# Optimization experiments

Measured on AMD Instinct MI355X. Metric: run time of the kernel, lower is better.

## Reference

```python
import jax, jax.numpy as jnp
import numpy as np

B, H, T, K, V = 2, 8, 2048, 128, 128


def setup_inputs() -> dict:
    key = jax.random.key(0)
    k1, k2, k3, k4, k5 = jax.random.split(key, 5)
    return {
        "q": jax.random.normal(k1, (B, H, T, K), dtype=jnp.float32),
        "k": jax.random.normal(k2, (B, H, T, K), dtype=jnp.float32),
        "v": jax.random.normal(k3, (B, H, T, V), dtype=jnp.float32),
        "i_gate": jax.random.normal(k4, (B, H, T), dtype=jnp.float32),
        "f_gate": jax.random.normal(k5, (B, H, T), dtype=jnp.float32),
    }


def reference(q, k, v, i_gate, f_gate):
    # Stabilized parallel mLSTM (same math as the chunked Triton kernel,
    # expressed in natural-log base instead of base-2).
    Bq, Hq, Tq, Kd = q.shape
    scale = Kd ** -0.5
    logf = jax.nn.log_sigmoid(f_gate)                      # [B,H,T]
    fc = jnp.cumsum(logf, axis=-1)                         # cumulative forget logits
    # log decay matrix: logD[t,s] = i[s] + (fc[t] - fc[s]) for s <= t
    logD = fc[..., :, None] - fc[..., None, :] + i_gate[..., None, :]  # [B,H,T,T]
    mask = jnp.tril(jnp.ones((Tq, Tq), dtype=bool))
    logD_masked = jnp.where(mask, logD, -jnp.inf)
    m = jnp.max(logD_masked, axis=-1)                      # row-wise stabilizer [B,H,T]
    D = jnp.where(mask, jnp.exp(logD - m[..., None]), 0.0) # stabilized decay matrix
    S = jnp.einsum("bhtk,bhsk->bhts", q, k) * scale * D    # gated scores
    norm = jnp.maximum(jnp.abs(jnp.sum(S, axis=-1)), jnp.exp(-m))  # [B,H,T]
    h = jnp.einsum("bhts,bhsv->bhtv", S, v) / norm[..., None]
    return h
```

## Files before the change

kernel.cpp:

```cpp
#include <hip/hip_runtime.h>

#define T_SEQ 2048
#define DHEAD 128
#define NBH 16
#define SCALE 0.08838834764831845f

typedef unsigned short u16;
typedef unsigned int u32;
typedef u16 u16x4 __attribute__((ext_vector_type(4)));
typedef u16 u16x8 __attribute__((ext_vector_type(8)));
typedef u32 u32x2 __attribute__((ext_vector_type(2)));
typedef short s16x4 __attribute__((ext_vector_type(4)));
typedef __bf16 bf16x8 __attribute__((ext_vector_type(8)));
typedef float f32x4 __attribute__((ext_vector_type(4)));

#define SFENCE() __builtin_amdgcn_sched_barrier(0)

__device__ __forceinline__ u16 f2bfu(float x) {
  union { float f; unsigned u; } c; c.f = x;
  unsigned u = c.u;
  u = u + 0x7FFFu + ((u >> 16) & 1u);
  return (u16)(u >> 16);
}

__device__ __forceinline__ bf16x8 ldsFrag(const u16* p) {
  u16x8 t = *(const u16x8*)p;
  return __builtin_bit_cast(bf16x8, t);
}

__device__ __forceinline__ f32x4 mfma16x16x16bf16(s16x4 a, s16x4 b, f32x4 c) {
#if __has_builtin(__builtin_amdgcn_mfma_f32_16x16x16bf16_1k)
  return __builtin_amdgcn_mfma_f32_16x16x16bf16_1k(a, b, c, 0, 0, 0);
#else
  asm("v_mfma_f32_16x16x16_bf16 %0, %1, %2, %0" : "+v"(c) : "v"(a), "v"(b));
  return c;
#endif
}

__device__ __forceinline__ void gld_lds16(const void* g, void* l) {
  __builtin_amdgcn_global_load_lds(
      (__attribute__((address_space(1))) const unsigned int*)g,
      (__attribute__((address_space(3))) unsigned int*)l, 16, 0, 0);
}

__global__ __launch_bounds__(1024) void gate_scan_kernel(
    const float* __restrict__ ig, const float* __restrict__ fg,
    float* __restrict__ a_out, float* __restrict__ c_out,
    float* __restrict__ fc_out)
{
  const int bh = blockIdx.x, tid = threadIdx.x;
  const int w = tid >> 6, lane = tid & 63;
  const int base = bh * T_SEQ + tid * 2;
  __shared__ float wsum[16];
  __shared__ float wmax[16];

  const float x0 = fg[base], x1 = fg[base + 1];
  const float ls0 = fminf(x0, 0.f) - log1pf(expf(-fabsf(x0)));
  const float ls1 = fminf(x1, 0.f) - log1pf(expf(-fabsf(x1)));
  const float s = ls0 + ls1;

  float sc = s;
#pragma unroll
  for (int off = 1; off < 64; off <<= 1) {
    const float t = __shfl_up(sc, off, 64);
    if (lane >= off) sc += t;
  }
  if (lane == 63) wsum[w] = sc;
  __syncthreads();
  float wo = 0.f;
#pragma unroll
  for (int i = 0; i < 15; ++i) if (i < w) wo += wsum[i];
  const float excl = wo + (sc - s);
  const float fc0 = excl + ls0;
  const float fc1 = excl + ls0 + ls1;
  fc_out[base] = fc0; fc_out[base + 1] = fc1;
  const float a0 = ig[base] - fc0;
  const float a1 = ig[base + 1] - fc1;
  a_out[base] = a0; a_out[base + 1] = a1;

  const float m = fmaxf(a0, a1);
  float mc = m;
#pragma unroll
  for (int off = 1; off < 64; off <<= 1) {
    const float t = __shfl_up(mc, off, 64);
    if (lane >= off) mc = fmaxf(mc, t);
  }
  if (lane == 63) wmax[w] = mc;
  __syncthreads();
  float wmo = -INFINITY;
#pragma unroll
  for (int i = 0; i < 15; ++i) if (i < w) wmo = fmaxf(wmo, wmax[i]);
  const float prev = __shfl_up(mc, 1, 64);
  float exclm = (lane > 0) ? prev : -INFINITY;
  exclm = fmaxf(exclm, wmo);
  c_out[base] = fmaxf(exclm, a0);
  c_out[base + 1] = fmaxf(exclm, m);
}

__global__ __launch_bounds__(256) void cvt_kv_kernel(
    const float* __restrict__ kk, const float* __restrict__ v,
    const float* __restrict__ ag, const float* __restrict__ cg,
    u16* __restrict__ kbf, u16* __restrict__ vt)
{
  const int bh = blockIdx.y, kt = blockIdx.x, tid = threadIdx.x;
  {
    const int r = tid >> 2;
    const int c0 = (tid & 3) * 32;
    const int row = kt * 64 + r;
    const float sc = __expf(ag[bh * T_SEQ + row] - cg[bh * T_SEQ + (row | 63)]);
    const float* sp = kk + ((size_t)bh * T_SEQ + row) * DHEAD + c0;
    u16* dp = kbf + ((size_t)bh * T_SEQ + row) * DHEAD + c0;
#pragma unroll
    for (int j = 0; j < 8; ++j) {
      const float4 x = *(const float4*)(sp + j * 4);
      u16x4 pq;
      pq[0] = f2bfu(x.x * sc); pq[1] = f2bfu(x.y * sc);
      pq[2] = f2bfu(x.z * sc); pq[3] = f2bfu(x.w * sc);
      *(u16x4*)(dp + j * 4) = pq;
    }
  }
  __shared__ __align__(16) u16 L[128 * 72];
  const int n0 = (tid & 31) * 4, k0 = (tid >> 5) * 8;
  const float* vp = v + ((size_t)bh * T_SEQ + kt * 64 + k0) * DHEAD + n0;
  u16 tv[4][8];
#pragma unroll
  for (int rr = 0; rr < 8; ++rr) {
    const float4 x = *(const float4*)(vp + rr * DHEAD);
    tv[0][rr] = f2bfu(x.x); tv[1][rr] = f2bfu(x.y);
    tv[2][rr] = f2bfu(x.z); tv[3][rr] = f2bfu(x.w);
  }
#pragma unroll
  for (int j = 0; j < 4; ++j) {
    u16x8 pq;
#pragma unroll
    for (int rr = 0; rr < 8; ++rr) pq[rr] = tv[j][rr];
    *(u16x8*)(&L[(n0 + j) * 72 + k0]) = pq;
  }
  __syncthreads();
  const int row = tid >> 1, s0 = (tid & 1) * 32;
  u16* op = vt + ((size_t)bh * DHEAD + row) * T_SEQ + kt * 64 + s0;
#pragma unroll
  for (int i = 0; i < 4; ++i)
    *(u16x8*)(op + i * 8) = *(const u16x8*)(&L[row * 72 + s0 + i * 8]);
}

template <bool FAST>
__global__ __launch_bounds__(1024, 4) void mlstm_fwd_kernel(
    const float* __restrict__ qg, const float* __restrict__ kxg,
    const float* __restrict__ vg,
    const u16* __restrict__ kbf, const u16* __restrict__ vtbf,
    const float* __restrict__ ag, const float* __restrict__ cg,
    const float* __restrict__ fcg, float* __restrict__ out)
{
  const int bx = (int)blockIdx.x;
  const int bh = bx & 15, p = bx >> 4;
  const int tid = (int)threadIdx.x;
  const int w = tid >> 6, lane = tid & 63;
  const int quad = lane >> 4, l16 = lane & 15;
  const int kg = w & 3, rq = w >> 2;

  const int qtA = 31 - p, qtB = p;
  const int nA = qtA + 1;

  __shared__ __align__(16) unsigned char SM[133120];
  u16* Kst = (u16*)SM;
  float* osh = (float*)(SM + 98304);
  float* rsh = (float*)(SM + 132096);

  const size_t hoff = (size_t)bh * T_SEQ * DHEAD;
  const int goff = bh * T_SEQ;

  auto barL = [&]() {
    asm volatile("s_waitcnt lgkmcnt(0)" ::: "memory");
    SFENCE();
    __builtin_amdgcn_s_barrier();
    SFENCE();
  };

  bf16x8 qf[4];
  auto loadQ = [&](int lqt) {
    const float* qp = qg + hoff + (size_t)(lqt * 64 + rq * 16 + l16) * DHEAD + quad * 8;
#pragma unroll
    for (int kc = 0; kc < 4; ++kc) {
      const float4 x0 = *(const float4*)(qp + kc * 32);
      const float4 x1 = *(const float4*)(qp + kc * 32 + 4);
      u16x8 t;
      t[0] = f2bfu(x0.x); t[1] = f2bfu(x0.y); t[2] = f2bfu(x0.z); t[3] = f2bfu(x0.w);
      t[4] = f2bfu(x1.x); t[5] = f2bfu(x1.y); t[6] = f2bfu(x1.z); t[7] = f2bfu(x1.w);
      qf[kc] = __builtin_bit_cast(bf16x8, t);
    }
  };

  f32x4 oa[8];
  float rsacc;
  auto zeroAcc = [&]() {
#pragma unroll
    for (int mt = 0; mt < 8; ++mt) oa[mt] = (f32x4){0.f, 0.f, 0.f, 0.f};
    rsacc = 0.f;
  };
  zeroAcc();

  const int skey = tid >> 4, sdb = (tid & 15) ^ (skey & 7);
  const u16* ksBase = kbf + (size_t)goff * DHEAD + (size_t)skey * DHEAD + sdb * 8;
  const int svn = tid >> 3, svk = (tid & 7) ^ (svn & 7);
  const u16* vsBase = vtbf + (size_t)bh * DHEAD * T_SEQ + (size_t)svn * T_SEQ + svk * 8;

  auto stage = [&](int st, int slot) {
    u16* KbL = Kst + slot * 16384;
    u16* VbL = Kst + slot * 16384 + 8192;
    if (FAST) {
      gld_lds16(ksBase + (size_t)st * 64 * DHEAD, KbL + w * 512);
      gld_lds16(vsBase + st * 64, VbL + w * 512);
    } else {
      const float ct = cg[goff + st * 64 + 63];
      const float* kp = kxg + hoff + (size_t)(st * 64) * DHEAD;
      const float* vp = vg + hoff + (size_t)(st * 64) * DHEAD;
      { const float scv = __expf(ag[goff + st * 64 + skey] - ct);
        const float4 x0 = *(const float4*)(kp + (size_t)skey * DHEAD + sdb * 8);
        const float4 x1 = *(const float4*)(kp + (size_t)skey * DHEAD + sdb * 8 + 4);
        u16x8 pk;
        pk[0] = f2bfu(x0.x * scv); pk[1] = f2bfu(x0.y * scv);
        pk[2] = f2bfu(x0.z * scv); pk[3] = f2bfu(x0.w * scv);
        pk[4] = f2bfu(x1.x * scv); pk[5] = f2bfu(x1.y * scv);
        pk[6] = f2bfu(x1.z * scv); pk[7] = f2bfu(x1.w * scv);
        *(u16x8*)(KbL + tid * 8) = pk; }
      { u16x8 pw;
#pragma unroll
        for (int rr = 0; rr < 8; ++rr)
          pw[rr] = f2bfu(vp[(size_t)(svk * 8 + rr) * DHEAD + svn]);
        *(u16x8*)(VbL + tid * 8) = pw; }
    }
  };
  auto stageSeq = [&](int seq, int slot) {
    stage(seq < nA ? seq : seq - nA, slot);
  };

  const int keyA = kg * 16 + l16;
  const int ksw  = l16 & 7;
  const int kbu  = kg * 2 + (quad >> 1);
  const int vbase = l16 * 64 + ((kbu ^ (l16 & 7)) * 8) + (quad & 1) * 4;

  auto computeStage = [&](int cqt, int st, int slot, float ccmax) {
    const u16* KbL = Kst + slot * 16384;
    const u16* VbL = Kst + slot * 16384 + 8192;

    f32x4 sa = (f32x4){0.f, 0.f, 0.f, 0.f};
#pragma unroll
    for (int kc = 0; kc < 4; ++kc) {
      const bf16x8 kf = ldsFrag(KbL + keyA * 128 + (((kc * 4 + quad) ^ ksw) * 8));
      sa = __builtin_amdgcn_mfma_f32_16x16x32_bf16(kf, qf[kc], sa, 0, 0, 0);
    }

    const float etile = SCALE * __expf(cg[goff + st * 64 + 63] - ccmax);
    float x0 = sa[0] * etile, x1 = sa[1] * etile;
    float x2 = sa[2] * etile, x3 = sa[3] * etile;
    if (st == cqt) {
      const int qr = rq * 16 + l16, kb0 = kg * 16 + quad * 4;
      if (kb0 + 0 > qr) x0 = 0.f;
      if (kb0 + 1 > qr) x1 = 0.f;
      if (kb0 + 2 > qr) x2 = 0.f;
      if (kb0 + 3 > qr) x3 = 0.f;
    }
    rsacc += (x0 + x1) + (x2 + x3);
    u32 plo, phi;
    asm("v_cvt_pk_bf16_f32 %0, %1, %2" : "=v"(plo) : "v"(x0), "v"(x1));
    asm("v_cvt_pk_bf16_f32 %0, %1, %2" : "=v"(phi) : "v"(x2), "v"(x3));
    const s16x4 pfr = __builtin_bit_cast(s16x4, (u32x2){plo, phi});

#pragma unroll
    for (int mt = 0; mt < 8; ++mt) {
      const s16x4 va = *(const s16x4*)(VbL + vbase + mt * 1024);
      oa[mt] = mfma16x16x16bf16(va, pfr, oa[mt]);
    }
  };

  auto epilogue = [&](int eqt, float ecmax) {
    float x = rsacc;
    x += __shfl_xor(x, 16, 64);
    x += __shfl_xor(x, 32, 64);
    if (lane < 16) rsh[kg * 64 + rq * 16 + lane] = x;
    barL();
    float inv = 0.f;
    if (kg == 3) {
      const int row = rq * 16 + l16;
      const float tot = rsh[row] + rsh[64 + row] + rsh[128 + row] + rsh[192 + row];
      const float nf = __expf(-(ecmax + fcg[goff + eqt * 64 + row]));
      inv = 1.f / fmaxf(fabsf(tot), nf);
    }
    for (int r = 0; r < 4; ++r) {
      if (kg == r) {
        const int row = rq * 16 + l16;
#pragma unroll
        for (int mt = 0; mt < 8; ++mt) {
          float* ap = osh + row * 132 + mt * 16 + quad * 4;
          f32x4 vv = oa[mt];
          if (r > 0) vv = vv + *(const f32x4*)ap;
          if (r == 3) vv = vv * inv;
          *(f32x4*)ap = vv;
        }
      }
      barL();
    }
    const int col = tid & 31, r0 = tid >> 5;
#pragma unroll
    for (int i = 0; i < 2; ++i) {
      const int row = r0 + 32 * i;
      const f32x4 vv = *(const f32x4*)(osh + row * 132 + col * 4);
      *(f32x4*)(out + hoff + (size_t)(eqt * 64 + row) * DHEAD + col * 4) = vv;
    }
  };

  int qt = qtA;
  float cmax = cg[goff + qtA * 64 + 63];
  loadQ(qtA);
  stageSeq(0, 0);
  stageSeq(1, 1);

  int sl = 0;
  for (int s = 0; s < 33; ++s) {
    if (s < 32) { asm volatile("s_waitcnt vmcnt(2)" ::: "memory"); }
    else        { asm volatile("s_waitcnt vmcnt(0)" ::: "memory"); }
    if (!FAST)  { asm volatile("s_waitcnt lgkmcnt(0)" ::: "memory"); }
    SFENCE();
    __builtin_amdgcn_s_barrier();
    SFENCE();

    if (s + 2 < 33) {
      const int sl2 = (sl >= 1) ? sl - 1 : 2;
      stageSeq(s + 2, sl2);
    }
    const int stq = (s < nA) ? s : s - nA;
    computeStage(qt, stq, sl, cmax);

    if (s == nA - 1) {
      loadQ(qtB);
      epilogue(qtA, cmax);
      zeroAcc();
      qt = qtB;
      cmax = cg[goff + qtB * 64 + 63];
    }
    sl = (sl == 2) ? 0 : sl + 1;
  }
  epilogue(qtB, cmax);
}

extern "C" void kernel_launch(void* const* d_in, const int* in_sizes, int n_in,
                              void* d_out, int out_size, void* d_ws, size_t ws_size,
                              hipStream_t stream) {
  const float* q  = (const float*)d_in[0];
  const float* k  = (const float*)d_in[1];
  const float* v  = (const float*)d_in[2];
  const float* ig = (const float*)d_in[3];
  const float* fg = (const float*)d_in[4];

  const size_t gate_bytes = (size_t)3 * NBH * T_SEQ * sizeof(float);
  const size_t kv_elems   = (size_t)NBH * T_SEQ * DHEAD;
  const bool fast = ws_size >= gate_bytes + 2 * kv_elems * sizeof(u16);

  float* a_ws  = (float*)d_ws;
  float* c_ws  = a_ws + NBH * T_SEQ;
  float* fc_ws = c_ws + NBH * T_SEQ;
  u16* kbf  = (u16*)((char*)d_ws + gate_bytes);
  u16* vtbf = kbf + kv_elems;

  gate_scan_kernel<<<dim3(NBH), dim3(1024), 0, stream>>>(ig, fg, a_ws, c_ws, fc_ws);
  if (fast) {
    cvt_kv_kernel<<<dim3(T_SEQ / 64, NBH), dim3(256), 0, stream>>>(
        k, v, a_ws, c_ws, kbf, vtbf);
    mlstm_fwd_kernel<true><<<dim3(256), dim3(1024), 0, stream>>>(
        q, k, v, kbf, vtbf, a_ws, c_ws, fc_ws, (float*)d_out);
  } else {
    mlstm_fwd_kernel<false><<<dim3(256), dim3(1024), 0, stream>>>(
        q, k, v, kbf, vtbf, a_ws, c_ws, fc_ws, (float*)d_out);
  }
}
```

Before: 146.8 us.

## Restructure K/V staging into double-buffered pairs with one barrier per pair

Replaces the three-slot rolling pipeline, which had a hand-tuned vmcnt wait and barrier per tile, with a ping-pong scheme that stages two key/value tiles per buffer and syncs once per pair. This halves the number of block-wide barriers in the main loop. Shared memory grows to four tile slots, so the output staging buffer is shrunk to 64 columns and the epilogue writes in two halves, which adds barriers there. The explicit waitcnt and sched_barrier control is dropped in favour of __syncthreads, so the compiler may insert more conservative waits and overlap global loads less.

```diff
diff --git a/kernel.cpp b/kernel.cpp
--- a/kernel.cpp
+++ b/kernel.cpp
@@ -13,8 +13,6 @@
 typedef short s16x4 __attribute__((ext_vector_type(4)));
 typedef __bf16 bf16x8 __attribute__((ext_vector_type(8)));
 typedef float f32x4 __attribute__((ext_vector_type(4)));
-
-#define SFENCE() __builtin_amdgcn_sched_barrier(0)
 
 __device__ __forceinline__ u16 f2bfu(float x) {
   union { float f; unsigned u; } c; c.f = x;
@@ -160,22 +158,15 @@
   const int kg = w & 3, rq = w >> 2;
 
   const int qtA = 31 - p, qtB = p;
-  const int nA = qtA + 1;
-
-  __shared__ __align__(16) unsigned char SM[133120];
+  const int nA = qtA + 1, nB = qtB + 1;
+
+  __shared__ __align__(16) unsigned char SM[148992];
   u16* Kst = (u16*)SM;
-  float* osh = (float*)(SM + 98304);
-  float* rsh = (float*)(SM + 132096);
+  float* osh = (float*)(SM + 131072);
+  float* rsh = (float*)(SM + 147968);
 
   const size_t hoff = (size_t)bh * T_SEQ * DHEAD;
   const int goff = bh * T_SEQ;
-
-  auto barL = [&]() {
-    asm volatile("s_waitcnt lgkmcnt(0)" ::: "memory");
-    SFENCE();
-    __builtin_amdgcn_s_barrier();
-    SFENCE();
-  };
 
   bf16x8 qf[4];
   auto loadQ = [&](int lqt) {
@@ -231,8 +222,9 @@
         *(u16x8*)(VbL + tid * 8) = pw; }
     }
   };
-  auto stageSeq = [&](int seq, int slot) {
-    stage(seq < nA ? seq : seq - nA, slot);
+  auto stagePair = [&](int s0, int lim, int pr) {
+    if (s0 < lim)     stage(s0,     pr * 2);
+    if (s0 + 1 < lim) stage(s0 + 1, pr * 2 + 1);
   };
 
   const int keyA = kg * 16 + l16;
@@ -279,7 +271,7 @@
     x += __shfl_xor(x, 16, 64);
     x += __shfl_xor(x, 32, 64);
     if (lane < 16) rsh[kg * 64 + rq * 16 + lane] = x;
-    barL();
+    __syncthreads();
     float inv = 0.f;
     if (kg == 3) {
       const int row = rq * 16 + l16;
@@ -287,61 +279,56 @@
       const float nf = __expf(-(ecmax + fcg[goff + eqt * 64 + row]));
       inv = 1.f / fmaxf(fabsf(tot), nf);
     }
-    for (int r = 0; r < 4; ++r) {
-      if (kg == r) {
-        const int row = rq * 16 + l16;
-#pragma unroll
-        for (int mt = 0; mt < 8; ++mt) {
-          float* ap = osh + row * 132 + mt * 16 + quad * 4;
-          f32x4 vv = oa[mt];
-          if (r > 0) vv = vv + *(const f32x4*)ap;
-          if (r == 3) vv = vv * inv;
-          *(f32x4*)ap = vv;
+    const int srow = tid >> 4, scol = tid & 15;
+#pragma unroll
+    for (int h = 0; h < 2; ++h) {
+      for (int r = 0; r < 4; ++r) {
+        if (kg == r) {
+          const int row = rq * 16 + l16;
+#pragma unroll
+          for (int ml = 0; ml < 4; ++ml) {
+            float* ap = osh + row * 66 + ml * 16 + quad * 4;
+            f32x4 vv = oa[h * 4 + ml];
+            if (r > 0) vv = vv + *(const f32x4*)ap;
+            if (r == 3) vv = vv * inv;
+            *(f32x4*)ap = vv;
+          }
         }
+        __syncthreads();
       }
-      barL();
-    }
-    const int col = tid & 31, r0 = tid >> 5;
-#pragma unroll
-    for (int i = 0; i < 2; ++i) {
-      const int row = r0 + 32 * i;
-      const f32x4 vv = *(const f32x4*)(osh + row * 132 + col * 4);
-      *(f32x4*)(out + hoff + (size_t)(eqt * 64 + row) * DHEAD + col * 4) = vv;
-    }
-  };
-
-  int qt = qtA;
+      {
+        const f32x4 vv = *(const f32x4*)(osh + srow * 66 + scol * 4);
+        *(f32x4*)(out + hoff + (size_t)(eqt * 64 + srow) * DHEAD + h * 64 + scol * 4) = vv;
+      }
+      __syncthreads();
+    }
+  };
+
+  int qt = qtA, n = nA;
   float cmax = cg[goff + qtA * 64 + 63];
   loadQ(qtA);
-  stageSeq(0, 0);
-  stageSeq(1, 1);
-
-  int sl = 0;
-  for (int s = 0; s < 33; ++s) {
-    if (s < 32) { asm volatile("s_waitcnt vmcnt(2)" ::: "memory"); }
-    else        { asm volatile("s_waitcnt vmcnt(0)" ::: "memory"); }
-    if (!FAST)  { asm volatile("s_waitcnt lgkmcnt(0)" ::: "memory"); }
-    SFENCE();
-    __builtin_amdgcn_s_barrier();
-    SFENCE();
-
-    if (s + 2 < 33) {
-      const int sl2 = (sl >= 1) ? sl - 1 : 2;
-      stageSeq(s + 2, sl2);
-    }
-    const int stq = (s < nA) ? s : s - nA;
-    computeStage(qt, stq, sl, cmax);
-
-    if (s == nA - 1) {
-      loadQ(qtB);
-      epilogue(qtA, cmax);
+  stagePair(0, nA, 0);
+  __syncthreads();
+
+  int pr = 0;
+  for (int phase = 0; phase < 2; ++phase) {
+    const int c = (n + 1) >> 1;
+    for (int g = 0; g < c; ++g) {
+      if (g + 1 < c)        stagePair(2 * (g + 1), n, pr ^ 1);
+      else if (phase == 0)  stagePair(0, nB, pr ^ 1);
+      computeStage(qt, 2 * g, pr * 2, cmax);
+      if (2 * g + 1 < n) computeStage(qt, 2 * g + 1, pr * 2 + 1, cmax);
+      __syncthreads();
+      pr ^= 1;
+    }
+    if (phase == 0) loadQ(qtB);
+    epilogue(qt, cmax);
+    if (phase == 0) {
       zeroAcc();
-      qt = qtB;
+      qt = qtB; n = nB;
       cmax = cg[goff + qtB * 64 + 63];
     }
-    sl = (sl == 2) ? 0 : sl + 1;
-  }
-  epilogue(qtB, cmax);
+  }
 }
 
 extern "C" void kernel_launch(void* const* d_in, const int* in_sizes, int n_in,
```

After: 154.9 us. +5.5%, slower.

## Read V fragments directly from global memory and double-buffer only K in LDS

Applied to the files above, without the earlier changes.

Stops staging V tiles through LDS. Each wave now loads its V^T fragments straight from global memory inside the PV MFMA loop, and the K pipeline drops from a 3-slot to a 2-slot double buffer with plain __syncthreads, which halves LDS use per block. Per-tile cumulative gate values are preloaded into a register once and fetched with wave shuffles instead of repeated global loads. The intent is to cut LDS footprint and staging traffic. The cost is exposed global-load latency on the V path, since it is no longer prefetched, and a less pipelined barrier schedule.

```diff
diff --git a/kernel.cpp b/kernel.cpp
--- a/kernel.cpp
+++ b/kernel.cpp
@@ -13,8 +13,6 @@
 typedef short s16x4 __attribute__((ext_vector_type(4)));
 typedef __bf16 bf16x8 __attribute__((ext_vector_type(8)));
 typedef float f32x4 __attribute__((ext_vector_type(4)));
-
-#define SFENCE() __builtin_amdgcn_sched_barrier(0)
 
 __device__ __forceinline__ u16 f2bfu(float x) {
   union { float f; unsigned u; } c; c.f = x;
@@ -162,20 +160,15 @@
   const int qtA = 31 - p, qtB = p;
   const int nA = qtA + 1;
 
-  __shared__ __align__(16) unsigned char SM[133120];
+  __shared__ __align__(16) unsigned char SM[67584];
   u16* Kst = (u16*)SM;
-  float* osh = (float*)(SM + 98304);
-  float* rsh = (float*)(SM + 132096);
+  float* osh = (float*)(SM + 32768);
+  float* rsh = (float*)(SM + 66560);
 
   const size_t hoff = (size_t)bh * T_SEQ * DHEAD;
   const int goff = bh * T_SEQ;
 
-  auto barL = [&]() {
-    asm volatile("s_waitcnt lgkmcnt(0)" ::: "memory");
-    SFENCE();
-    __builtin_amdgcn_s_barrier();
-    SFENCE();
-  };
+  const float cgl = cg[goff + (lane & 31) * 64 + 63];
 
   bf16x8 qf[4];
   auto loadQ = [&](int lqt) {
@@ -202,47 +195,33 @@
 
   const int skey = tid >> 4, sdb = (tid & 15) ^ (skey & 7);
   const u16* ksBase = kbf + (size_t)goff * DHEAD + (size_t)skey * DHEAD + sdb * 8;
-  const int svn = tid >> 3, svk = (tid & 7) ^ (svn & 7);
-  const u16* vsBase = vtbf + (size_t)bh * DHEAD * T_SEQ + (size_t)svn * T_SEQ + svk * 8;
-
-  auto stage = [&](int st, int slot) {
-    u16* KbL = Kst + slot * 16384;
-    u16* VbL = Kst + slot * 16384 + 8192;
+
+  auto stage = [&](int st, int b) {
+    u16* KbL = Kst + b * 8192;
     if (FAST) {
       gld_lds16(ksBase + (size_t)st * 64 * DHEAD, KbL + w * 512);
-      gld_lds16(vsBase + st * 64, VbL + w * 512);
     } else {
       const float ct = cg[goff + st * 64 + 63];
-      const float* kp = kxg + hoff + (size_t)(st * 64) * DHEAD;
-      const float* vp = vg + hoff + (size_t)(st * 64) * DHEAD;
-      { const float scv = __expf(ag[goff + st * 64 + skey] - ct);
-        const float4 x0 = *(const float4*)(kp + (size_t)skey * DHEAD + sdb * 8);
-        const float4 x1 = *(const float4*)(kp + (size_t)skey * DHEAD + sdb * 8 + 4);
-        u16x8 pk;
-        pk[0] = f2bfu(x0.x * scv); pk[1] = f2bfu(x0.y * scv);
-        pk[2] = f2bfu(x0.z * scv); pk[3] = f2bfu(x0.w * scv);
-        pk[4] = f2bfu(x1.x * scv); pk[5] = f2bfu(x1.y * scv);
-        pk[6] = f2bfu(x1.z * scv); pk[7] = f2bfu(x1.w * scv);
-        *(u16x8*)(KbL + tid * 8) = pk; }
-      { u16x8 pw;
-#pragma unroll
-        for (int rr = 0; rr < 8; ++rr)
-          pw[rr] = f2bfu(vp[(size_t)(svk * 8 + rr) * DHEAD + svn]);
-        *(u16x8*)(VbL + tid * 8) = pw; }
-    }
-  };
-  auto stageSeq = [&](int seq, int slot) {
-    stage(seq < nA ? seq : seq - nA, slot);
+      const float* kp = kxg + hoff + (size_t)(st * 64 + skey) * DHEAD + sdb * 8;
+      const float scv = __expf(ag[goff + st * 64 + skey] - ct);
+      const float4 x0 = *(const float4*)kp;
+      const float4 x1 = *(const float4*)(kp + 4);
+      u16x8 pk;
+      pk[0] = f2bfu(x0.x * scv); pk[1] = f2bfu(x0.y * scv);
+      pk[2] = f2bfu(x0.z * scv); pk[3] = f2bfu(x0.w * scv);
+      pk[4] = f2bfu(x1.x * scv); pk[5] = f2bfu(x1.y * scv);
+      pk[6] = f2bfu(x1.z * scv); pk[7] = f2bfu(x1.w * scv);
+      *(u16x8*)(KbL + tid * 8) = pk;
+    }
   };
 
   const int keyA = kg * 16 + l16;
   const int ksw  = l16 & 7;
-  const int kbu  = kg * 2 + (quad >> 1);
-  const int vbase = l16 * 64 + ((kbu ^ (l16 & 7)) * 8) + (quad & 1) * 4;
-
-  auto computeStage = [&](int cqt, int st, int slot, float ccmax) {
-    const u16* KbL = Kst + slot * 16384;
-    const u16* VbL = Kst + slot * 16384 + 8192;
+  const u16* vTh = vtbf + (size_t)bh * DHEAD * T_SEQ + (size_t)l16 * T_SEQ
+                 + kg * 16 + quad * 4;
+
+  auto computeStage = [&](int cqt, int st, int b, float ccmax) {
+    const u16* KbL = Kst + b * 8192;
 
     f32x4 sa = (f32x4){0.f, 0.f, 0.f, 0.f};
 #pragma unroll
@@ -251,7 +230,8 @@
       sa = __builtin_amdgcn_mfma_f32_16x16x32_bf16(kf, qf[kc], sa, 0, 0, 0);
     }
 
-    const float etile = SCALE * __expf(cg[goff + st * 64 + 63] - ccmax);
+    const float ct = __shfl(cgl, st, 64);
+    const float etile = SCALE * __expf(ct - ccmax);
     float x0 = sa[0] * etile, x1 = sa[1] * etile;
     float x2 = sa[2] * etile, x3 = sa[3] * etile;
     if (st == cqt) {
@@ -267,9 +247,21 @@
     asm("v_cvt_pk_bf16_f32 %0, %1, %2" : "=v"(phi) : "v"(x2), "v"(x3));
     const s16x4 pfr = __builtin_bit_cast(s16x4, (u32x2){plo, phi});
 
+    const u16* vSt = vTh + st * 64;
 #pragma unroll
     for (int mt = 0; mt < 8; ++mt) {
-      const s16x4 va = *(const s16x4*)(VbL + vbase + mt * 1024);
+      s16x4 va;
+      if (FAST) {
+        va = *(const s16x4*)(vSt + (size_t)mt * 16 * T_SEQ);
+      } else {
+        const int kb = st * 64 + kg * 16 + quad * 4;
+        const int vd = mt * 16 + l16;
+        u16x4 tv;
+#pragma unroll
+        for (int j = 0; j < 4; ++j)
+          tv[j] = f2bfu(vg[hoff + (size_t)(kb + j) * DHEAD + vd]);
+        va = __builtin_bit_cast(s16x4, tv);
+      }
       oa[mt] = mfma16x16x16bf16(va, pfr, oa[mt]);
     }
   };
@@ -279,7 +271,7 @@
     x += __shfl_xor(x, 16, 64);
     x += __shfl_xor(x, 32, 64);
     if (lane < 16) rsh[kg * 64 + rq * 16 + lane] = x;
-    barL();
+    __syncthreads();
     float inv = 0.f;
     if (kg == 3) {
       const int row = rq * 16 + l16;
@@ -299,7 +291,7 @@
           *(f32x4*)ap = vv;
         }
       }
-      barL();
+      __syncthreads();
     }
     const int col = tid & 31, r0 = tid >> 5;
 #pragma unroll
@@ -308,38 +300,29 @@
       const f32x4 vv = *(const f32x4*)(osh + row * 132 + col * 4);
       *(f32x4*)(out + hoff + (size_t)(eqt * 64 + row) * DHEAD + col * 4) = vv;
     }
+    __syncthreads();
   };
 
   int qt = qtA;
-  float cmax = cg[goff + qtA * 64 + 63];
+  float cmax = __shfl(cgl, qtA, 64);
   loadQ(qtA);
-  stageSeq(0, 0);
-  stageSeq(1, 1);
-
-  int sl = 0;
-  for (int s = 0; s < 33; ++s) {
-    if (s < 32) { asm volatile("s_waitcnt vmcnt(2)" ::: "memory"); }
-    else        { asm volatile("s_waitcnt vmcnt(0)" ::: "memory"); }
-    if (!FAST)  { asm volatile("s_waitcnt lgkmcnt(0)" ::: "memory"); }
-    SFENCE();
-    __builtin_amdgcn_s_barrier();
-    SFENCE();
-
-    if (s + 2 < 33) {
-      const int sl2 = (sl >= 1) ? sl - 1 : 2;
-      stageSeq(s + 2, sl2);
-    }
-    const int stq = (s < nA) ? s : s - nA;
-    computeStage(qt, stq, sl, cmax);
-
-    if (s == nA - 1) {
+  stage(0, 0);
+  __syncthreads();
+
+  for (int it = 0; it < 33; ++it) {
+    if (it < 32) {
+      const int nx = it + 1;
+      stage(nx < nA ? nx : nx - nA, nx & 1);
+    }
+    computeStage(qt, (it < nA) ? it : it - nA, it & 1, cmax);
+    __syncthreads();
+    if (it == nA - 1) {
       loadQ(qtB);
       epilogue(qtA, cmax);
       zeroAcc();
       qt = qtB;
-      cmax = cg[goff + qtB * 64 + 63];
-    }
-    sl = (sl == 2) ? 0 : sl + 1;
+      cmax = __shfl(cgl, qtB, 64);
+    }
   }
   epilogue(qtB, cmax);
 }
```

Measured after the change: 235.8 us. +60.6%, slower.
